# Kernel optimization log

Hardware: AMD Instinct MI355X
Metric: run time of the kernel (lower is better)

The kernel has to match this reference:

```python
import jax, jax.numpy as jnp
import numpy as np

N = 50000      # nodes
E = 800000     # edges (avg degree 16)
IN = 128       # in_features
H = 4          # num_heads
OUT = 32       # out_features per head
NEG_SLOPE = 0.2


def setup_inputs() -> dict:
    key = jax.random.key(0)
    k1, k2, k3, k4 = jax.random.split(key, 4)
    h = jax.random.normal(k1, (N, IN), dtype=jnp.float32)
    edge_index = jax.random.randint(k2, (2, E), 0, N, dtype=jnp.int32)
    # xavier-ish init scales
    W = jax.random.normal(k3, (H, IN, OUT), dtype=jnp.float32) * np.float32(np.sqrt(2.0 / (IN + OUT)))
    a = jax.random.normal(k4, (H, 2 * OUT), dtype=jnp.float32) * np.float32(np.sqrt(2.0 / (2 * OUT)))
    return {"h": h, "edge_index": edge_index, "W": W, "a": a}


def reference(h, edge_index, W, a):
    src, dst = edge_index[0], edge_index[1]
    # project per head: [N, H, OUT]
    h_proj = jnp.einsum('ni,hio->nho', h, W)
    # score = leaky_relu(a . [Wh_src || Wh_dst]) ; split a to avoid materializing the concat
    a_src, a_dst = a[:, :OUT], a[:, OUT:]
    s_src = jnp.einsum('nho,ho->nh', h_proj, a_src)   # [N, H]
    s_dst = jnp.einsum('nho,ho->nh', h_proj, a_dst)   # [N, H]
    score = jax.nn.leaky_relu(s_src[src] + s_dst[dst], negative_slope=NEG_SLOPE)  # [E, H]
    # sparse softmax over incoming edges of each dst node
    smax = jax.ops.segment_max(score, dst, num_segments=N)          # [N, H]
    smax = jnp.where(jnp.isfinite(smax), smax, jnp.float32(-1e9))   # nodes with no in-edges
    score_exp = jnp.exp(score - smax[dst])                          # [E, H]
    denom = jax.ops.segment_sum(score_exp, dst, num_segments=N)     # [N, H]
    denom = jnp.maximum(denom, jnp.float32(1e-16))
    alpha = score_exp / denom[dst]                                  # [E, H]
    # weighted aggregation (dropout is identity in eval mode)
    h_src = h_proj[src]                                             # [E, H, OUT]
    h_out = jax.ops.segment_sum(alpha[:, :, None] * h_src, dst, num_segments=N)  # [N, H, OUT]
    h_out = h_out.reshape(N, H * OUT)  # concat=True
    return jax.nn.elu(h_out)
```

## Files before the change

kernel.cpp:

```cpp
#include <hip/hip_runtime.h>

#define NEG_SLOPE 0.2f

typedef __attribute__((ext_vector_type(8))) short short8;
typedef __attribute__((ext_vector_type(4))) float floatx4;

__device__ __forceinline__ unsigned f2bf(float x) {
  unsigned u = __float_as_uint(x);
  unsigned r = ((u >> 16) & 1u) + 0x7fffu;
  return (u + r) >> 16;
}
__device__ __forceinline__ float bf2f(unsigned hi16) {
  return __uint_as_float(hi16 << 16);
}

__global__ __launch_bounds__(256) void k_prep(const float* __restrict__ W,
                                              uint4* __restrict__ gWf) {
  const int u = blockIdx.x * 256 + threadIdx.x;
  if (u >= 2048) return;
  int ln = u & 63;
  int kc = (u >> 6) & 3;
  int ct = u >> 8;
  int n = ct * 16 + (ln & 15);
  int kb = kc * 32 + (ln >> 4) * 8;
  int head = n >> 5;
  const float* src = W + head * 4096 + (size_t)kb * 32 + (n & 31);
  unsigned hi[4], lo[4];
#pragma unroll
  for (int jj = 0; jj < 4; ++jj) {
    float w0 = src[(2 * jj) * 32];
    float w1 = src[(2 * jj + 1) * 32];
    unsigned h0 = f2bf(w0), h1 = f2bf(w1);
    unsigned l0 = f2bf(w0 - bf2f(h0)), l1 = f2bf(w1 - bf2f(h1));
    hi[jj] = h0 | (h1 << 16);
    lo[jj] = l0 | (l1 << 16);
  }
  gWf[u] = make_uint4(hi[0], hi[1], hi[2], hi[3]);
  gWf[2048 + u] = make_uint4(lo[0], lo[1], lo[2], lo[3]);
}

__global__ __launch_bounds__(256) void k_gemm(const float* __restrict__ h,
                                              const uint4* __restrict__ gWf,
                                              const float* __restrict__ a,
                                              const int* __restrict__ ei,
                                              unsigned short* __restrict__ hp16,
                                              float* __restrict__ ssrc,
                                              float* __restrict__ sdst,
                                              int* __restrict__ gcntT,
                                              int N, int E, int NB1, int NB2) {
  __shared__ unsigned lds_u[16384];
  __shared__ int cnt[256];
  const int tid = threadIdx.x;

  if (blockIdx.x < NB1) {
    for (int i = tid; i < NB2; i += 256) cnt[i] = 0;
    __syncthreads();
    const int e0 = blockIdx.x * 4096;
#pragma unroll
    for (int j = 0; j < 16; ++j) {
      int e = e0 + j * 256 + tid;
      if (e < E) atomicAdd(&cnt[ei[E + e] >> 8], 1);
    }
    __syncthreads();
    for (int i = tid; i < NB2; i += 256)
      gcntT[(size_t)i * NB1 + blockIdx.x] = cnt[i];
  }

  const int lane = tid & 63;
  const int wv = tid >> 6;
  const int quad = lane >> 4;
  const int l16 = lane & 15;

  for (int u = tid; u < 4096; u += 256)
    *(uint4*)&lds_u[u * 4] = gWf[u];

  const int row0 = blockIdx.x * 64;
  const int r = row0 + wv * 16 + l16;
  short8 Ah[4], Al[4];
#pragma unroll
  for (int kc = 0; kc < 4; ++kc) {
    float v[8];
    if (r < N) {
      float4 fa = *(const float4*)&h[(size_t)r * 128 + kc * 32 + quad * 8];
      float4 fb = *(const float4*)&h[(size_t)r * 128 + kc * 32 + quad * 8 + 4];
      v[0] = fa.x; v[1] = fa.y; v[2] = fa.z; v[3] = fa.w;
      v[4] = fb.x; v[5] = fb.y; v[6] = fb.z; v[7] = fb.w;
    } else {
#pragma unroll
      for (int j = 0; j < 8; ++j) v[j] = 0.f;
    }
#pragma unroll
    for (int j = 0; j < 8; ++j) {
      unsigned hi = f2bf(v[j]);
      Ah[kc][j] = (short)hi;
      Al[kc][j] = (short)f2bf(v[j] - bf2f(hi));
    }
  }
  __syncthreads();

  floatx4 C[8];
#pragma unroll
  for (int ct = 0; ct < 8; ++ct) {
    floatx4 c = {0.f, 0.f, 0.f, 0.f};
#pragma unroll
    for (int kc = 0; kc < 4; ++kc) {
      int bidx = ((ct * 4 + kc) * 64 + lane) * 4;
      short8 Bh, Bl;
      *(uint4*)&Bh = *(const uint4*)&lds_u[bidx];
      *(uint4*)&Bl = *(const uint4*)&lds_u[8192 + bidx];
      c = __builtin_amdgcn_mfma_f32_16x16x32_bf16(Ah[kc], Bh, c, 0, 0, 0);
      c = __builtin_amdgcn_mfma_f32_16x16x32_bf16(Al[kc], Bh, c, 0, 0, 0);
      c = __builtin_amdgcn_mfma_f32_16x16x32_bf16(Ah[kc], Bl, c, 0, 0, 0);
    }
    C[ct] = c;
  }
  __syncthreads();

  float* epi = (float*)lds_u;
#pragma unroll
  for (int ct = 0; ct < 8; ++ct) {
#pragma unroll
    for (int reg = 0; reg < 4; ++reg) {
      int rr = wv * 16 + quad * 4 + reg;
      epi[rr * 132 + ct * 16 + l16] = C[ct][reg];
    }
  }
  __syncthreads();

  const int row_l = tid >> 2;
  const int hh = tid & 3;
  const int rg = row0 + row_l;
  if (rg < N) {
    const float* rowp = &epi[row_l * 132 + hh * 32];
    float ss = 0.f, sd = 0.f;
    unsigned pka[16];
#pragma unroll
    for (int e = 0; e < 8; ++e) {
      float4 c4 = *(const float4*)&rowp[e * 4];
      float4 as = *(const float4*)&a[hh * 64 + e * 4];
      float4 ad = *(const float4*)&a[hh * 64 + 32 + e * 4];
      ss += c4.x * as.x + c4.y * as.y + c4.z * as.z + c4.w * as.w;
      sd += c4.x * ad.x + c4.y * ad.y + c4.z * ad.z + c4.w * ad.w;
      pka[e * 2] = f2bf(c4.x) | (f2bf(c4.y) << 16);
      pka[e * 2 + 1] = f2bf(c4.z) | (f2bf(c4.w) << 16);
    }
    unsigned short* dst = &hp16[(size_t)rg * 128 + hh * 32];
    *(uint4*)(dst) = make_uint4(pka[0], pka[1], pka[2], pka[3]);
    *(uint4*)(dst + 8) = make_uint4(pka[4], pka[5], pka[6], pka[7]);
    *(uint4*)(dst + 16) = make_uint4(pka[8], pka[9], pka[10], pka[11]);
    *(uint4*)(dst + 24) = make_uint4(pka[12], pka[13], pka[14], pka[15]);
    ssrc[(size_t)rg * 4 + hh] = ss;
    sdst[(size_t)rg * 4 + hh] = sd;
  }
}

__global__ __launch_bounds__(256) void k_scan_col(int* __restrict__ gcntT,
                                                  int* __restrict__ btot, int NB1) {
  __shared__ int lds[256];
  const int tid = threadIdx.x;
  int* col = gcntT + (size_t)blockIdx.x * NB1;
  int carry = 0;
  for (int base = 0; base < NB1; base += 256) {
    int i = base + tid;
    int v = (i < NB1) ? col[i] : 0;
    lds[tid] = v;
    __syncthreads();
    for (int off = 1; off < 256; off <<= 1) {
      int t = (tid >= off) ? lds[tid - off] : 0;
      __syncthreads();
      lds[tid] += t;
      __syncthreads();
    }
    if (i < NB1) col[i] = carry + lds[tid] - v;
    carry += lds[255];
    __syncthreads();
  }
  if (tid == 0) btot[blockIdx.x] = carry;
}

__global__ __launch_bounds__(256) void k_bin(const int* __restrict__ ei,
                                             const int* __restrict__ gcntT,
                                             const int* __restrict__ btot,
                                             uint2* __restrict__ gpairs,
                                             int E, int NB1, int NB2) {
  __shared__ uint2 stage[4096];
  __shared__ int cnt[256], start[256], cur[256], gbase[256];
  __shared__ int lds[256];
  const int tid = threadIdx.x;
  const int e0 = blockIdx.x * 4096;
  int bt = (tid < NB2) ? btot[tid] : 0;
  lds[tid] = bt;
  __syncthreads();
  for (int off = 1; off < 256; off <<= 1) {
    int t = (tid >= off) ? lds[tid - off] : 0;
    __syncthreads();
    lds[tid] += t;
    __syncthreads();
  }
  const int bbase_t = lds[tid] - bt;
  for (int i = tid; i < NB2; i += 256) cnt[i] = 0;
  __syncthreads();
  int sarr[16], darr[16];
#pragma unroll
  for (int j = 0; j < 16; ++j) {
    int e = e0 + j * 256 + tid;
    if (e < E) {
      sarr[j] = ei[e];
      darr[j] = ei[E + e];
      atomicAdd(&cnt[darr[j] >> 8], 1);
    } else {
      darr[j] = -1;
    }
  }
  __syncthreads();
  {
    int s = (tid < NB2) ? cnt[tid] : 0;
    lds[tid] = s;
    __syncthreads();
    for (int off = 1; off < 256; off <<= 1) {
      int t = (tid >= off) ? lds[tid - off] : 0;
      __syncthreads();
      lds[tid] += t;
      __syncthreads();
    }
    if (tid < NB2) {
      start[tid] = lds[tid] - s;
      cur[tid] = lds[tid] - s;
      gbase[tid] = gcntT[(size_t)tid * NB1 + blockIdx.x] + bbase_t;
    }
  }
  __syncthreads();
#pragma unroll
  for (int j = 0; j < 16; ++j) {
    if (darr[j] >= 0) {
      int b = darr[j] >> 8;
      int pos = atomicAdd(&cur[b], 1);
      stage[pos] = make_uint2((unsigned)sarr[j], (unsigned)darr[j]);
    }
  }
  __syncthreads();
  const int total = start[NB2 - 1] + cnt[NB2 - 1];
  for (int u = tid; u < total; u += 256) {
    uint2 pr = stage[u];
    int b = (int)(pr.y >> 8);
    gpairs[gbase[b] + (u - start[b])] = pr;
  }
}

__global__ __launch_bounds__(256) void k_build(const int* __restrict__ btot,
                                               const uint2* __restrict__ gpairs,
                                               int* __restrict__ csr_src,
                                               int* __restrict__ offs, int N, int NB2) {
  __shared__ int cnt2[256], start2[256], cur2[256];
  __shared__ int lds[256];
  __shared__ int bshare[2];
  __shared__ int srcsort[8192];
  const int tid = threadIdx.x;
  const int b = blockIdx.x;
  int bt = (tid < NB2) ? btot[tid] : 0;
  lds[tid] = bt;
  __syncthreads();
  for (int off = 1; off < 256; off <<= 1) {
    int t = (tid >= off) ? lds[tid - off] : 0;
    __syncthreads();
    lds[tid] += t;
    __syncthreads();
  }
  if (tid == b) {
    bshare[0] = lds[tid] - bt;
    bshare[1] = bt;
  }
  cnt2[tid] = 0;
  __syncthreads();
  const int base = bshare[0];
  const int size = bshare[1];
  const int d0 = b << 8;
  const int ndst = min(256, N - d0);
  for (int u = tid; u < size; u += 256)
    atomicAdd(&cnt2[(int)gpairs[base + u].y - d0], 1);
  __syncthreads();
  {
    int s = cnt2[tid];
    lds[tid] = s;
    __syncthreads();
    for (int off = 1; off < 256; off <<= 1) {
      int t = (tid >= off) ? lds[tid - off] : 0;
      __syncthreads();
      lds[tid] += t;
      __syncthreads();
    }
    start2[tid] = lds[tid] - s;
    cur2[tid] = lds[tid] - s;
  }
  __syncthreads();
  for (int u = tid; u < size; u += 256) {
    uint2 pr = gpairs[base + u];
    int pos = atomicAdd(&cur2[(int)pr.y - d0], 1);
    srcsort[pos] = (int)pr.x;
  }
  __syncthreads();
  for (int u = tid; u < size; u += 256) csr_src[base + u] = srcsort[u];
  if (tid < ndst) offs[d0 + tid] = base + start2[tid] + cnt2[tid];
}

__global__ __launch_bounds__(256) void k_agg(const int* __restrict__ offs,
                                             const int* __restrict__ csr_src,
                                             const float* __restrict__ ssrc,
                                             const float* __restrict__ sdst,
                                             const uint4* __restrict__ hp4,
                                             float* __restrict__ out, int N) {
  const int t = blockIdx.x * 256 + threadIdx.x;
  const int d = t >> 4;
  if (d >= N) return;
  const int l = threadIdx.x & 15;
  const int hh = l >> 2;
  const int beg = (d == 0) ? 0 : offs[d - 1];
  const int end = offs[d];
  const float sdh = sdst[(size_t)d * 4 + hh];

  float den[4] = {0.f, 0.f, 0.f, 0.f};
  float acc[8];
#pragma unroll
  for (int j = 0; j < 8; ++j) acc[j] = 0.f;

  int p = beg;
  for (; p + 3 < end; p += 4) {
    int s[4];
    float sc[4];
    uint4 v[4];
#pragma unroll
    for (int q = 0; q < 4; ++q) s[q] = csr_src[p + q];
#pragma unroll
    for (int q = 0; q < 4; ++q) {
      sc[q] = ssrc[(size_t)s[q] * 4 + hh] + sdh;
      v[q] = hp4[(size_t)s[q] * 16 + l];
    }
#pragma unroll
    for (int q = 0; q < 4; ++q) {
      float x = sc[q];
      x = x >= 0.f ? x : NEG_SLOPE * x;
      float w = __expf(x);
      den[q] += w;
      acc[0] = fmaf(w, bf2f(v[q].x & 0xffffu), acc[0]);
      acc[1] = fmaf(w, bf2f(v[q].x >> 16), acc[1]);
      acc[2] = fmaf(w, bf2f(v[q].y & 0xffffu), acc[2]);
      acc[3] = fmaf(w, bf2f(v[q].y >> 16), acc[3]);
      acc[4] = fmaf(w, bf2f(v[q].z & 0xffffu), acc[4]);
      acc[5] = fmaf(w, bf2f(v[q].z >> 16), acc[5]);
      acc[6] = fmaf(w, bf2f(v[q].w & 0xffffu), acc[6]);
      acc[7] = fmaf(w, bf2f(v[q].w >> 16), acc[7]);
    }
  }
  for (; p < end; ++p) {
    int s0 = csr_src[p];
    float sc0 = ssrc[(size_t)s0 * 4 + hh] + sdh;
    uint4 v0 = hp4[(size_t)s0 * 16 + l];
    sc0 = sc0 >= 0.f ? sc0 : NEG_SLOPE * sc0;
    float w0 = __expf(sc0);
    den[0] += w0;
    acc[0] = fmaf(w0, bf2f(v0.x & 0xffffu), acc[0]);
    acc[1] = fmaf(w0, bf2f(v0.x >> 16), acc[1]);
    acc[2] = fmaf(w0, bf2f(v0.y & 0xffffu), acc[2]);
    acc[3] = fmaf(w0, bf2f(v0.y >> 16), acc[3]);
    acc[4] = fmaf(w0, bf2f(v0.z & 0xffffu), acc[4]);
    acc[5] = fmaf(w0, bf2f(v0.z >> 16), acc[5]);
    acc[6] = fmaf(w0, bf2f(v0.w & 0xffffu), acc[6]);
    acc[7] = fmaf(w0, bf2f(v0.w >> 16), acc[7]);
  }
  float rden = 1.f / fmaxf((den[0] + den[1]) + (den[2] + den[3]), 1e-16f);
  float o[8];
#pragma unroll
  for (int j = 0; j < 8; ++j) {
    float x = acc[j] * rden;
    o[j] = x > 0.f ? x : expm1f(x);
  }
  float* dst = &out[(size_t)d * 128 + l * 8];
  *(float4*)dst = make_float4(o[0], o[1], o[2], o[3]);
  *(float4*)(dst + 4) = make_float4(o[4], o[5], o[6], o[7]);
}

extern "C" void kernel_launch(void* const* d_in, const int* in_sizes, int n_in,
                              void* d_out, int out_size, void* d_ws, size_t ws_size,
                              hipStream_t stream) {
  const float* h = (const float*)d_in[0];
  const int* ei = (const int*)d_in[1];
  const float* W = (const float*)d_in[2];
  const float* a = (const float*)d_in[3];
  float* out = (float*)d_out;
  const int N = in_sizes[0] / 128;
  const int E = in_sizes[1] / 2;
  const int NB2 = (N + 255) >> 8;
  const int NB1 = (E + 4095) / 4096;

  char* ws = (char*)d_ws;
  uint4* gWf = (uint4*)ws;
  unsigned short* hp16 = (unsigned short*)(gWf + 4096);
  uint2* gpairs = (uint2*)(hp16 + (size_t)N * 128);
  float* ssrc = (float*)(gpairs + (size_t)E);
  float* sdst = ssrc + (size_t)N * 4;
  int* gcntT = (int*)(sdst + (size_t)N * 4);
  int* btot = gcntT + (size_t)NB2 * NB1;
  int* offs = btot + NB2;
  int* csr_src = offs + N;

  k_prep<<<8, 256, 0, stream>>>(W, gWf);
  k_gemm<<<(N + 63) / 64, 256, 0, stream>>>(h, gWf, a, ei, hp16, ssrc, sdst,
                                            gcntT, N, E, NB1, NB2);
  k_scan_col<<<NB2, 256, 0, stream>>>(gcntT, btot, NB1);
  k_bin<<<NB1, 256, 0, stream>>>(ei, gcntT, btot, gpairs, E, NB1, NB2);
  k_build<<<NB2, 256, 0, stream>>>(btot, gpairs, csr_src, offs, N, NB2);
  k_agg<<<(N * 16 + 255) / 256, 256, 0, stream>>>(offs, csr_src, ssrc, sdst,
                                                  (const uint4*)hp16, out, N);
}
```

Before: 163.6 us.

## Replace counting-sort prefix scans with fixed-capacity buckets and atomic cursors

Each destination bucket now gets a fixed region of BCAP slots, and per-block offsets come from a global atomicAdd on a bucket cursor. This removes the histogram pass folded into the GEMM, the column-scan kernel, and the redundant bucket-total scans in k_bin and k_build. CSR offsets become explicit (begin,end) pairs because buckets are no longer contiguous. It drops one launch and several serial LDS scans, but if more than 8192 edges land in one bucket it overflows the buffer, and the edge order inside a node now depends on scheduling.

```diff
diff --git a/kernel.cpp b/kernel.cpp
--- a/kernel.cpp
+++ b/kernel.cpp
@@ -1,6 +1,7 @@
 #include <hip/hip_runtime.h>
 
 #define NEG_SLOPE 0.2f
+#define BCAP 8192
 
 typedef __attribute__((ext_vector_type(8))) short short8;
 typedef __attribute__((ext_vector_type(4))) float floatx4;
@@ -15,7 +16,9 @@
 }
 
 __global__ __launch_bounds__(256) void k_prep(const float* __restrict__ W,
-                                              uint4* __restrict__ gWf) {
+                                              uint4* __restrict__ gWf,
+                                              int* __restrict__ bcur, int NB2) {
+  if (blockIdx.x == 0 && threadIdx.x < NB2) bcur[threadIdx.x] = 0;
   const int u = blockIdx.x * 256 + threadIdx.x;
   if (u >= 2048) return;
   int ln = u & 63;
@@ -42,30 +45,11 @@
 __global__ __launch_bounds__(256) void k_gemm(const float* __restrict__ h,
                                               const uint4* __restrict__ gWf,
                                               const float* __restrict__ a,
-                                              const int* __restrict__ ei,
                                               unsigned short* __restrict__ hp16,
                                               float* __restrict__ ssrc,
-                                              float* __restrict__ sdst,
-                                              int* __restrict__ gcntT,
-                                              int N, int E, int NB1, int NB2) {
+                                              float* __restrict__ sdst, int N) {
   __shared__ unsigned lds_u[16384];
-  __shared__ int cnt[256];
   const int tid = threadIdx.x;
-
-  if (blockIdx.x < NB1) {
-    for (int i = tid; i < NB2; i += 256) cnt[i] = 0;
-    __syncthreads();
-    const int e0 = blockIdx.x * 4096;
-#pragma unroll
-    for (int j = 0; j < 16; ++j) {
-      int e = e0 + j * 256 + tid;
-      if (e < E) atomicAdd(&cnt[ei[E + e] >> 8], 1);
-    }
-    __syncthreads();
-    for (int i = tid; i < NB2; i += 256)
-      gcntT[(size_t)i * NB1 + blockIdx.x] = cnt[i];
-  }
-
   const int lane = tid & 63;
   const int wv = tid >> 6;
   const int quad = lane >> 4;
@@ -154,50 +138,15 @@
   }
 }
 
-__global__ __launch_bounds__(256) void k_scan_col(int* __restrict__ gcntT,
-                                                  int* __restrict__ btot, int NB1) {
-  __shared__ int lds[256];
-  const int tid = threadIdx.x;
-  int* col = gcntT + (size_t)blockIdx.x * NB1;
-  int carry = 0;
-  for (int base = 0; base < NB1; base += 256) {
-    int i = base + tid;
-    int v = (i < NB1) ? col[i] : 0;
-    lds[tid] = v;
-    __syncthreads();
-    for (int off = 1; off < 256; off <<= 1) {
-      int t = (tid >= off) ? lds[tid - off] : 0;
-      __syncthreads();
-      lds[tid] += t;
-      __syncthreads();
-    }
-    if (i < NB1) col[i] = carry + lds[tid] - v;
-    carry += lds[255];
-    __syncthreads();
-  }
-  if (tid == 0) btot[blockIdx.x] = carry;
-}
-
 __global__ __launch_bounds__(256) void k_bin(const int* __restrict__ ei,
-                                             const int* __restrict__ gcntT,
-                                             const int* __restrict__ btot,
+                                             int* __restrict__ bcur,
                                              uint2* __restrict__ gpairs,
-                                             int E, int NB1, int NB2) {
+                                             int E, int NB2) {
   __shared__ uint2 stage[4096];
   __shared__ int cnt[256], start[256], cur[256], gbase[256];
   __shared__ int lds[256];
   const int tid = threadIdx.x;
   const int e0 = blockIdx.x * 4096;
-  int bt = (tid < NB2) ? btot[tid] : 0;
-  lds[tid] = bt;
-  __syncthreads();
-  for (int off = 1; off < 256; off <<= 1) {
-    int t = (tid >= off) ? lds[tid - off] : 0;
-    __syncthreads();
-    lds[tid] += t;
-    __syncthreads();
-  }
-  const int bbase_t = lds[tid] - bt;
   for (int i = tid; i < NB2; i += 256) cnt[i] = 0;
   __syncthreads();
   int sarr[16], darr[16];
@@ -226,7 +175,7 @@
     if (tid < NB2) {
       start[tid] = lds[tid] - s;
       cur[tid] = lds[tid] - s;
-      gbase[tid] = gcntT[(size_t)tid * NB1 + blockIdx.x] + bbase_t;
+      gbase[tid] = s ? atomicAdd(&bcur[tid], s) : 0;
     }
   }
   __syncthreads();
@@ -243,39 +192,25 @@
   for (int u = tid; u < total; u += 256) {
     uint2 pr = stage[u];
     int b = (int)(pr.y >> 8);
-    gpairs[gbase[b] + (u - start[b])] = pr;
-  }
-}
-
-__global__ __launch_bounds__(256) void k_build(const int* __restrict__ btot,
+    gpairs[(size_t)b * BCAP + gbase[b] + (u - start[b])] = pr;
+  }
+}
+
+__global__ __launch_bounds__(256) void k_build(const int* __restrict__ bcur,
                                                const uint2* __restrict__ gpairs,
                                                int* __restrict__ csr_src,
-                                               int* __restrict__ offs, int N, int NB2) {
+                                               int2* __restrict__ offs2, int N) {
   __shared__ int cnt2[256], start2[256], cur2[256];
   __shared__ int lds[256];
-  __shared__ int bshare[2];
-  __shared__ int srcsort[8192];
+  __shared__ int srcsort[BCAP];
   const int tid = threadIdx.x;
   const int b = blockIdx.x;
-  int bt = (tid < NB2) ? btot[tid] : 0;
-  lds[tid] = bt;
-  __syncthreads();
-  for (int off = 1; off < 256; off <<= 1) {
-    int t = (tid >= off) ? lds[tid - off] : 0;
-    __syncthreads();
-    lds[tid] += t;
-    __syncthreads();
-  }
-  if (tid == b) {
-    bshare[0] = lds[tid] - bt;
-    bshare[1] = bt;
-  }
-  cnt2[tid] = 0;
-  __syncthreads();
-  const int base = bshare[0];
-  const int size = bshare[1];
+  const size_t base = (size_t)b * BCAP;
+  const int size = bcur[b];
   const int d0 = b << 8;
   const int ndst = min(256, N - d0);
+  cnt2[tid] = 0;
+  __syncthreads();
   for (int u = tid; u < size; u += 256)
     atomicAdd(&cnt2[(int)gpairs[base + u].y - d0], 1);
   __syncthreads();
@@ -300,10 +235,13 @@
   }
   __syncthreads();
   for (int u = tid; u < size; u += 256) csr_src[base + u] = srcsort[u];
-  if (tid < ndst) offs[d0 + tid] = base + start2[tid] + cnt2[tid];
-}
-
-__global__ __launch_bounds__(256) void k_agg(const int* __restrict__ offs,
+  if (tid < ndst) {
+    int beg = (int)base + start2[tid];
+    offs2[d0 + tid] = make_int2(beg, beg + cnt2[tid]);
+  }
+}
+
+__global__ __launch_bounds__(256) void k_agg(const int2* __restrict__ offs2,
                                              const int* __restrict__ csr_src,
                                              const float* __restrict__ ssrc,
                                              const float* __restrict__ sdst,
@@ -314,8 +252,8 @@
   if (d >= N) return;
   const int l = threadIdx.x & 15;
   const int hh = l >> 2;
-  const int beg = (d == 0) ? 0 : offs[d - 1];
-  const int end = offs[d];
+  const int2 be = offs2[d];
+  const int beg = be.x, end = be.y;
   const float sdh = sdst[(size_t)d * 4 + hh];
 
   float den[4] = {0.f, 0.f, 0.f, 0.f};
@@ -396,19 +334,16 @@
   uint4* gWf = (uint4*)ws;
   unsigned short* hp16 = (unsigned short*)(gWf + 4096);
   uint2* gpairs = (uint2*)(hp16 + (size_t)N * 128);
-  float* ssrc = (float*)(gpairs + (size_t)E);
+  int2* offs2 = (int2*)(gpairs + (size_t)NB2 * BCAP);
+  float* ssrc = (float*)(offs2 + N);
   float* sdst = ssrc + (size_t)N * 4;
-  int* gcntT = (int*)(sdst + (size_t)N * 4);
-  int* btot = gcntT + (size_t)NB2 * NB1;
-  int* offs = btot + NB2;
-  int* csr_src = offs + N;
-
-  k_prep<<<8, 256, 0, stream>>>(W, gWf);
-  k_gemm<<<(N + 63) / 64, 256, 0, stream>>>(h, gWf, a, ei, hp16, ssrc, sdst,
-                                            gcntT, N, E, NB1, NB2);
-  k_scan_col<<<NB2, 256, 0, stream>>>(gcntT, btot, NB1);
-  k_bin<<<NB1, 256, 0, stream>>>(ei, gcntT, btot, gpairs, E, NB1, NB2);
-  k_build<<<NB2, 256, 0, stream>>>(btot, gpairs, csr_src, offs, N, NB2);
-  k_agg<<<(N * 16 + 255) / 256, 256, 0, stream>>>(offs, csr_src, ssrc, sdst,
+  int* bcur = (int*)(sdst + (size_t)N * 4);
+  int* csr_src = bcur + NB2;
+
+  k_prep<<<8, 256, 0, stream>>>(W, gWf, bcur, NB2);
+  k_gemm<<<(N + 63) / 64, 256, 0, stream>>>(h, gWf, a, hp16, ssrc, sdst, N);
+  k_bin<<<NB1, 256, 0, stream>>>(ei, bcur, gpairs, E, NB2);
+  k_build<<<NB2, 256, 0, stream>>>(bcur, gpairs, csr_src, offs2, N);
+  k_agg<<<(N * 16 + 255) / 256, 256, 0, stream>>>(offs2, csr_src, ssrc, sdst,
                                                   (const uint4*)hp16, out, N);
 }
```

New measurement: 159.7 us. 2.4% less time.
